# Performance work log

Hardware: AMD Instinct MI355X
Metric: run time of the kernel (lower is better)

The kernel has to match this reference:

```python
import jax, jax.numpy as jnp
import numpy as np

B, T, L_CTX = 64, 150, 256
H = 512   # decoder_num_hidden
E = 512   # target_embedding_size
V = 1000  # target_vocab_size


def setup_inputs() -> dict:
    key = jax.random.key(0)
    ks = jax.random.split(key, 10)
    s = 0.05
    return {
        "cnn_feats": jax.random.normal(ks[0], (B, L_CTX, H), dtype=jnp.float32),
        "seq": jax.random.randint(ks[1], (B, T), 0, V, dtype=jnp.int32),
        "embed_table": jax.random.normal(ks[2], (V, E), dtype=jnp.float32) * s,
        "W_ih": jax.random.normal(ks[3], (4 * H, E), dtype=jnp.float32) * s,
        "b_ih": jnp.zeros((4 * H,), dtype=jnp.float32),
        "W_hh": jax.random.normal(ks[4], (4 * H, H), dtype=jnp.float32) * s,
        "b_hh": jnp.zeros((4 * H,), dtype=jnp.float32),
        "W_hm": jax.random.normal(ks[5], (H, H), dtype=jnp.float32) * s,
        "W_om": jax.random.normal(ks[6], (H, 2 * H), dtype=jnp.float32) * s,
        "W_logit": jax.random.normal(ks[7], (V, H), dtype=jnp.float32) * s,
        "b_logit": jnp.zeros((V,), dtype=jnp.float32),
    }


def reference(cnn_feats, seq, embed_table, W_ih, b_ih, W_hh, b_hh,
              W_hm, W_om, W_logit, b_logit):
    # Single-layer LSTMCell decoder with per-step attention (eval mode, dropout=0).
    def step(carry, it):
        h, c = carry                      # [B,H] each
        xt = jax.nn.relu(embed_table[it])  # [B,E]
        gates = xt @ W_ih.T + b_ih + h @ W_hh.T + b_hh  # [B,4H]
        i, f, g, o = jnp.split(gates, 4, axis=1)
        c2 = jax.nn.sigmoid(f) * c + jax.nn.sigmoid(i) * jnp.tanh(g)
        h2 = jax.nn.sigmoid(o) * jnp.tanh(c2)
        mapped = h2 @ W_hm.T              # [B,H]
        attn = jnp.einsum("blh,bh->bl", cnn_feats, mapped)
        w = jax.nn.softmax(attn, axis=1)
        ctx = jnp.einsum("bl,blh->bh", w, cnn_feats)
        out = jnp.concatenate([ctx, h2], axis=1) @ W_om.T  # [B,H]
        logp = jax.nn.log_softmax(out @ W_logit.T + b_logit, axis=1)
        return (h2, c2), logp

    bsz = cnn_feats.shape[0]
    h0 = jnp.zeros((bsz, W_hh.shape[1]), dtype=cnn_feats.dtype)
    c0 = jnp.zeros_like(h0)
    _, outs = jax.lax.scan(step, (h0, c0), seq.T)  # outs: [T,B,V]
    return outs.transpose(1, 0, 2)  # [B,T,V]
```

## Files before the change

### kernel.cpp

```cpp
#include <hip/hip_runtime.h>
#include <math.h>

#define B_  64
#define T_  150
#define L_  256
#define H_  512
#define E_  512
#define V_  1000
#define G4_ 2048
#define DB_ 16
#define HCB 32

typedef _Float16 f16;
typedef f16   f16x8 __attribute__((ext_vector_type(8)));
typedef f16   f16x4 __attribute__((ext_vector_type(4)));
typedef float f32x4 __attribute__((ext_vector_type(4)));
typedef unsigned long long ull;

__device__ __forceinline__ float sigmf(float x) { return 1.0f / (1.0f + expf(-x)); }

__global__ __launch_bounds__(512) void decoder_mfma(
    const int*   __restrict__ seq,
    const float* __restrict__ G,
    const float* __restrict__ Whh,
    ull*  __restrict__ xh,
    int*  __restrict__ tags,
    float* __restrict__ hbuf)
{
    __shared__ f16   hlds[64][520];
    __shared__ float glds[64][132];
    __shared__ float csh[64][36];

    const int tid = threadIdx.x;
    const int bb  = blockIdx.x;
    const int ln  = tid & 63;
    const int wv  = tid >> 6;
    const int mh  = wv >> 2;
    const int nt2 = wv & 3;

    f16x8 bfr[2][16];
    #pragma unroll
    for (int j = 0; j < 2; ++j) {
        const int n = 2 * nt2 + j;
        const int grow = (n >> 1) * H_ + bb * HCB + (n & 1) * 16 + (ln & 15);
        #pragma unroll
        for (int kt = 0; kt < 16; ++kt) {
            const int k0 = kt * 32 + (ln >> 4) * 8;
            float4 w0 = *(const float4*)(Whh + (size_t)grow * H_ + k0);
            float4 w1 = *(const float4*)(Whh + (size_t)grow * H_ + k0 + 4);
            bfr[j][kt] = (f16x8){(f16)w0.x, (f16)w0.y, (f16)w0.z, (f16)w0.w,
                                 (f16)w1.x, (f16)w1.y, (f16)w1.z, (f16)w1.w};
        }
    }
    for (int e = tid; e < 64 * 520 / 4; e += 512) ((ull*)hlds)[e] = 0ull;
    for (int e = tid; e < 64 * 36; e += 512) ((float*)csh)[e] = 0.f;
    __syncthreads();

    const int cb = tid >> 3, cg = tid & 7;

    for (int t = 0; t < T_; ++t) {
        const int v = seq[cb * T_ + t];
        const float* gp = G + (size_t)v * G4_ + bb * HCB + cg * 4;
        float4 gq0 = *(const float4*)(gp);
        float4 gq1 = *(const float4*)(gp + H_);
        float4 gq2 = *(const float4*)(gp + 2 * H_);
        float4 gq3 = *(const float4*)(gp + 3 * H_);

        if (t > 0) {
            if (tid < DB_) {
                while (__hip_atomic_load(&tags[tid], __ATOMIC_RELAXED,
                                         __HIP_MEMORY_SCOPE_AGENT) < t) {}
            }
            __syncthreads();
            const ull* src = xh + (size_t)(t & 1) * 64 * 128;
            ull v0[8], v1[8];
            #pragma unroll
            for (int it = 0; it < 8; ++it) {
                const int e = tid + it * 512;
                const int b = e >> 6, s = e & 63;
                v0[it] = __hip_atomic_load(&src[b * 128 + 2 * s], __ATOMIC_RELAXED,
                                           __HIP_MEMORY_SCOPE_AGENT);
                v1[it] = __hip_atomic_load(&src[b * 128 + 2 * s + 1], __ATOMIC_RELAXED,
                                           __HIP_MEMORY_SCOPE_AGENT);
            }
            #pragma unroll
            for (int it = 0; it < 8; ++it) {
                const int e = tid + it * 512;
                const int b = e >> 6, s = e & 63;
                ull* dst = (ull*)&hlds[b][s * 8];
                dst[0] = v0[it]; dst[1] = v1[it];
            }
            __syncthreads();
        }

        f32x4 acc00 = {0.f,0.f,0.f,0.f}, acc01 = {0.f,0.f,0.f,0.f};
        f32x4 acc10 = {0.f,0.f,0.f,0.f}, acc11 = {0.f,0.f,0.f,0.f};
        #pragma unroll
        for (int kt = 0; kt < 16; ++kt) {
            const int ko = kt * 32 + (ln >> 4) * 8;
            f16x8 a0 = *(const f16x8*)&hlds[(2 * mh)     * 16 + (ln & 15)][ko];
            f16x8 a1 = *(const f16x8*)&hlds[(2 * mh + 1) * 16 + (ln & 15)][ko];
            acc00 = __builtin_amdgcn_mfma_f32_16x16x32_f16(a0, bfr[0][kt], acc00, 0, 0, 0);
            acc01 = __builtin_amdgcn_mfma_f32_16x16x32_f16(a0, bfr[1][kt], acc01, 0, 0, 0);
            acc10 = __builtin_amdgcn_mfma_f32_16x16x32_f16(a1, bfr[0][kt], acc10, 0, 0, 0);
            acc11 = __builtin_amdgcn_mfma_f32_16x16x32_f16(a1, bfr[1][kt], acc11, 0, 0, 0);
        }
        {
            const int r0 = (2 * mh) * 16 + (ln >> 4) * 4;
            const int r1 = (2 * mh + 1) * 16 + (ln >> 4) * 4;
            const int c0 = (2 * nt2) * 16 + (ln & 15);
            const int c1 = (2 * nt2 + 1) * 16 + (ln & 15);
            #pragma unroll
            for (int i = 0; i < 4; ++i) {
                glds[r0 + i][c0] = acc00[i];
                glds[r0 + i][c1] = acc01[i];
                glds[r1 + i][c0] = acc10[i];
                glds[r1 + i][c1] = acc11[i];
            }
        }
        __syncthreads();

        {
            float4 Gi = *(const float4*)&glds[cb][cg * 4];
            float4 Gf = *(const float4*)&glds[cb][32 + cg * 4];
            float4 Gg = *(const float4*)&glds[cb][64 + cg * 4];
            float4 Go = *(const float4*)&glds[cb][96 + cg * 4];
            float4 cold = *(const float4*)&csh[cb][cg * 4];
            float gi[4] = {Gi.x + gq0.x, Gi.y + gq0.y, Gi.z + gq0.z, Gi.w + gq0.w};
            float gf[4] = {Gf.x + gq1.x, Gf.y + gq1.y, Gf.z + gq1.z, Gf.w + gq1.w};
            float gg[4] = {Gg.x + gq2.x, Gg.y + gq2.y, Gg.z + gq2.z, Gg.w + gq2.w};
            float go[4] = {Go.x + gq3.x, Go.y + gq3.y, Go.z + gq3.z, Go.w + gq3.w};
            float cl[4] = {cold.x, cold.y, cold.z, cold.w};
            float4 cnew, hnew;
            f16x4 hp;
            #pragma unroll
            for (int i = 0; i < 4; ++i) {
                float c2 = sigmf(gf[i]) * cl[i] + sigmf(gi[i]) * tanhf(gg[i]);
                float h2 = sigmf(go[i]) * tanhf(c2);
                ((float*)&cnew)[i] = c2;
                ((float*)&hnew)[i] = h2;
                hp[i] = (f16)h2;
            }
            *(float4*)&csh[cb][cg * 4] = cnew;
            *(float4*)&hbuf[((size_t)t * 64 + cb) * H_ + bb * HCB + cg * 4] = hnew;
            __hip_atomic_store(
                &xh[(size_t)((t + 1) & 1) * 64 * 128 + cb * 128 + bb * 8 + cg],
                __builtin_bit_cast(ull, hp),
                __ATOMIC_RELAXED, __HIP_MEMORY_SCOPE_AGENT);
        }
        __syncthreads();
        if (tid == 0)
            __hip_atomic_store(&tags[bb], t + 1, __ATOMIC_RELAXED,
                               __HIP_MEMORY_SCOPE_AGENT);
    }
}

template<bool RELU_A, bool REMAP>
__global__ __launch_bounds__(256) void gemm16_nt(
    const float* __restrict__ A1, const float* __restrict__ A2,
    const float* __restrict__ Bm,
    const float* __restrict__ bias1, const float* __restrict__ bias2,
    float* __restrict__ C, int M, int N, int KA)
{
    __shared__ f16 As[64][40];
    __shared__ f16 Bs[64][40];
    const int tid = threadIdx.x;
    const int m0 = blockIdx.x * 64, n0 = blockIdx.y * 64;
    const int ln = tid & 63, wv = tid >> 6;
    const int lr = tid >> 2, lc8 = (tid & 3) * 8;
    const int K = A2 ? 2 * KA : KA;
    f32x4 acc[4] = {};

    for (int kb = 0; kb < K; kb += 32) {
        const float* Ap; int kk;
        if (kb < KA) { Ap = A1; kk = kb; } else { Ap = A2; kk = kb - KA; }
        int gm = m0 + lr;
        float4 a0 = make_float4(0.f, 0.f, 0.f, 0.f), a1 = a0;
        if (gm < M) {
            a0 = *(const float4*)(Ap + (size_t)gm * KA + kk + lc8);
            a1 = *(const float4*)(Ap + (size_t)gm * KA + kk + lc8 + 4);
        }
        if (RELU_A) {
            a0.x = fmaxf(a0.x, 0.f); a0.y = fmaxf(a0.y, 0.f);
            a0.z = fmaxf(a0.z, 0.f); a0.w = fmaxf(a0.w, 0.f);
            a1.x = fmaxf(a1.x, 0.f); a1.y = fmaxf(a1.y, 0.f);
            a1.z = fmaxf(a1.z, 0.f); a1.w = fmaxf(a1.w, 0.f);
        }
        f16x8 av = {(f16)a0.x, (f16)a0.y, (f16)a0.z, (f16)a0.w,
                    (f16)a1.x, (f16)a1.y, (f16)a1.z, (f16)a1.w};
        *(f16x8*)&As[lr][lc8] = av;

        int gn = n0 + lr;
        float4 b0 = make_float4(0.f, 0.f, 0.f, 0.f), b1 = b0;
        if (gn < N) {
            b0 = *(const float4*)(Bm + (size_t)gn * K + kb + lc8);
            b1 = *(const float4*)(Bm + (size_t)gn * K + kb + lc8 + 4);
        }
        f16x8 bv = {(f16)b0.x, (f16)b0.y, (f16)b0.z, (f16)b0.w,
                    (f16)b1.x, (f16)b1.y, (f16)b1.z, (f16)b1.w};
        *(f16x8*)&Bs[lr][lc8] = bv;
        __syncthreads();

        f16x8 af = *(const f16x8*)&As[wv * 16 + (ln & 15)][(ln >> 4) * 8];
        #pragma unroll
        for (int ntt = 0; ntt < 4; ++ntt) {
            f16x8 bf = *(const f16x8*)&Bs[ntt * 16 + (ln & 15)][(ln >> 4) * 8];
            acc[ntt] = __builtin_amdgcn_mfma_f32_16x16x32_f16(af, bf, acc[ntt], 0, 0, 0);
        }
        __syncthreads();
    }

    #pragma unroll
    for (int ntt = 0; ntt < 4; ++ntt) {
        #pragma unroll
        for (int i = 0; i < 4; ++i) {
            int gm = m0 + wv * 16 + (ln >> 4) * 4 + i;
            int gn = n0 + ntt * 16 + (ln & 15);
            if (gm < M && gn < N) {
                float v = acc[ntt][i];
                if (bias1) v += bias1[gn];
                if (bias2) v += bias2[gn];
                size_t row = REMAP ? ((size_t)(gm & 63) * T_ + (gm >> 6)) : (size_t)gm;
                C[row * (size_t)N + gn] = v;
            }
        }
    }
}

__global__ __launch_bounds__(256) void gemm_nt(
    const float* __restrict__ A, size_t lda, size_t azs,
    const float* __restrict__ Bm, size_t ldb, size_t bzs,
    float* __restrict__ C, size_t ldc, size_t czs, int M, int N, int K)
{
    A  += blockIdx.z * azs;
    Bm += blockIdx.z * bzs;
    C  += blockIdx.z * czs;
    __shared__ __align__(16) float As[16][68];
    __shared__ __align__(16) float Bs[16][68];
    const int tid = threadIdx.x;
    const int m0 = blockIdx.x * 64;
    const int n0 = blockIdx.y * 64;
    const int lr = tid >> 2;
    const int lc = (tid & 3) << 2;
    const int tm = (tid & 15) << 2;
    const int tn = (tid >> 4) << 2;
    float acc[4][4] = {};

    for (int kb = 0; kb < K; kb += 16) {
        float4 a4 = make_float4(0.f, 0.f, 0.f, 0.f);
        int gm = m0 + lr;
        if (gm < M) a4 = *(const float4*)(A + (size_t)gm * lda + kb + lc);
        As[lc + 0][lr] = a4.x; As[lc + 1][lr] = a4.y;
        As[lc + 2][lr] = a4.z; As[lc + 3][lr] = a4.w;

        float4 b4 = make_float4(0.f, 0.f, 0.f, 0.f);
        int gn = n0 + lr;
        if (gn < N) b4 = *(const float4*)(Bm + (size_t)gn * ldb + kb + lc);
        Bs[lc + 0][lr] = b4.x; Bs[lc + 1][lr] = b4.y;
        Bs[lc + 2][lr] = b4.z; Bs[lc + 3][lr] = b4.w;
        __syncthreads();

        #pragma unroll
        for (int k = 0; k < 16; ++k) {
            float4 av = *(const float4*)&As[k][tm];
            float4 bv = *(const float4*)&Bs[k][tn];
            float af[4] = {av.x, av.y, av.z, av.w};
            float bf[4] = {bv.x, bv.y, bv.z, bv.w};
            #pragma unroll
            for (int i = 0; i < 4; ++i)
                #pragma unroll
                for (int j = 0; j < 4; ++j)
                    acc[i][j] += af[i] * bf[j];
        }
        __syncthreads();
    }

    #pragma unroll
    for (int i = 0; i < 4; ++i) {
        int gm = m0 + tm + i;
        if (gm >= M) continue;
        #pragma unroll
        for (int j = 0; j < 4; ++j) {
            int gn = n0 + tn + j;
            if (gn >= N) continue;
            C[(size_t)gm * ldc + gn] = acc[i][j];
        }
    }
}

__global__ __launch_bounds__(256) void gemm_nn(
    const float* __restrict__ A, size_t lda, size_t azs,
    const float* __restrict__ Bm, size_t ldb, size_t bzs,
    float* __restrict__ C, size_t ldc, size_t czs, int M, int N, int K)
{
    A  += blockIdx.z * azs;
    Bm += blockIdx.z * bzs;
    C  += blockIdx.z * czs;
    __shared__ __align__(16) float As[16][68];
    __shared__ __align__(16) float Bs[16][68];
    const int tid = threadIdx.x;
    const int m0 = blockIdx.x * 64;
    const int n0 = blockIdx.y * 64;
    const int lr = tid >> 2;
    const int lc = (tid & 3) << 2;
    const int br = tid >> 4;
    const int bc = (tid & 15) << 2;
    const int tm = (tid & 15) << 2;
    const int tn = (tid >> 4) << 2;
    float acc[4][4] = {};

    for (int kb = 0; kb < K; kb += 16) {
        float4 a4 = make_float4(0.f, 0.f, 0.f, 0.f);
        int gm = m0 + lr;
        if (gm < M) a4 = *(const float4*)(A + (size_t)gm * lda + kb + lc);
        As[lc + 0][lr] = a4.x; As[lc + 1][lr] = a4.y;
        As[lc + 2][lr] = a4.z; As[lc + 3][lr] = a4.w;

        float4 b4 = make_float4(0.f, 0.f, 0.f, 0.f);
        if (n0 + bc < N) b4 = *(const float4*)(Bm + (size_t)(kb + br) * ldb + n0 + bc);
        Bs[br][bc + 0] = b4.x; Bs[br][bc + 1] = b4.y;
        Bs[br][bc + 2] = b4.z; Bs[br][bc + 3] = b4.w;
        __syncthreads();

        #pragma unroll
        for (int k = 0; k < 16; ++k) {
            float4 av = *(const float4*)&As[k][tm];
            float4 bv = *(const float4*)&Bs[k][tn];
            float af[4] = {av.x, av.y, av.z, av.w};
            float bf[4] = {bv.x, bv.y, bv.z, bv.w};
            #pragma unroll
            for (int i = 0; i < 4; ++i)
                #pragma unroll
                for (int j = 0; j < 4; ++j)
                    acc[i][j] += af[i] * bf[j];
        }
        __syncthreads();
    }

    #pragma unroll
    for (int i = 0; i < 4; ++i) {
        int gm = m0 + tm + i;
        if (gm >= M) continue;
        #pragma unroll
        for (int j = 0; j < 4; ++j) {
            int gn = n0 + tn + j;
            if (gn >= N) continue;
            C[(size_t)gm * ldc + gn] = acc[i][j];
        }
    }
}

__global__ __launch_bounds__(256) void att_softmax(float* __restrict__ att, int nrows)
{
    const int tid = threadIdx.x, lane = tid & 63, wave = tid >> 6;
    const int row = blockIdx.x * 4 + wave;
    if (row >= nrows) return;
    float4* p = (float4*)(att + (size_t)row * L_);
    float4 sc = p[lane];
    float mx = fmaxf(fmaxf(sc.x, sc.y), fmaxf(sc.z, sc.w));
    #pragma unroll
    for (int off = 32; off; off >>= 1) mx = fmaxf(mx, __shfl_xor(mx, off));
    float e0 = expf(sc.x - mx), e1 = expf(sc.y - mx);
    float e2 = expf(sc.z - mx), e3 = expf(sc.w - mx);
    float s = e0 + e1 + e2 + e3;
    #pragma unroll
    for (int off = 32; off; off >>= 1) s += __shfl_xor(s, off);
    float inv = 1.f / s;
    p[lane] = make_float4(e0 * inv, e1 * inv, e2 * inv, e3 * inv);
}

__global__ __launch_bounds__(256) void logsoftmax_k(float* __restrict__ out)
{
    const int row = blockIdx.x;
    float* p = out + (size_t)row * V_;
    const int tid = threadIdx.x, lane = tid & 63, wave = tid >> 6;
    __shared__ float red[8];

    float vals[4];
    int n = 0;
    float mx = -INFINITY;
    for (int v = tid; v < V_; v += 256) { vals[n] = p[v]; mx = fmaxf(mx, vals[n]); ++n; }
    #pragma unroll
    for (int off = 32; off; off >>= 1) mx = fmaxf(mx, __shfl_xor(mx, off));
    if (lane == 0) red[wave] = mx;
    __syncthreads();
    mx = fmaxf(fmaxf(red[0], red[1]), fmaxf(red[2], red[3]));

    float s = 0.f;
    for (int i = 0; i < n; ++i) s += expf(vals[i] - mx);
    #pragma unroll
    for (int off = 32; off; off >>= 1) s += __shfl_xor(s, off);
    if (lane == 0) red[4 + wave] = s;
    __syncthreads();
    s = red[4] + red[5] + red[6] + red[7];

    const float lse = mx + logf(s);
    n = 0;
    for (int v = tid; v < V_; v += 256) { p[v] = vals[n] - lse; ++n; }
}

extern "C" void kernel_launch(void* const* d_in, const int* in_sizes, int n_in,
                              void* d_out, int out_size, void* d_ws, size_t ws_size,
                              hipStream_t stream)
{
    const float* cnn     = (const float*)d_in[0];
    const int*   seq     = (const int*)d_in[1];
    const float* embed   = (const float*)d_in[2];
    const float* W_ih    = (const float*)d_in[3];
    const float* b_ih    = (const float*)d_in[4];
    const float* W_hh    = (const float*)d_in[5];
    const float* b_hh    = (const float*)d_in[6];
    const float* W_hm    = (const float*)d_in[7];
    const float* W_om    = (const float*)d_in[8];
    const float* W_logit = (const float*)d_in[9];
    const float* b_logit = (const float*)d_in[10];
    float* out = (float*)d_out;

    float* ws = (float*)d_ws;
    float* G    = ws;
    float* hbuf = G + (size_t)V_ * G4_;
    float* outv = hbuf + (size_t)B_ * T_ * H_;
    ull*   xh   = (ull*)(outv + (size_t)B_ * T_ * H_);
    int*   tags = (int*)(xh + 2 * 64 * 128);
    float* mapped = out;
    float* attb   = out + (size_t)B_ * T_ * H_;

    hipMemsetAsync(tags, 0, DB_ * sizeof(int), stream);

    gemm16_nt<true, false><<<dim3(16, 32), 256, 0, stream>>>(
        embed, nullptr, W_ih, b_ih, b_hh, G, V_, G4_, E_);

    decoder_mfma<<<DB_, 512, 0, stream>>>(seq, G, W_hh, xh, tags, hbuf);

    gemm16_nt<false, false><<<dim3(150, 8), 256, 0, stream>>>(
        hbuf, nullptr, W_hm, nullptr, nullptr, mapped, B_ * T_, H_, H_);
    gemm_nt<<<dim3(3, 4, 64), 256, 0, stream>>>(
        mapped, (size_t)B_ * H_, H_,
        cnn, H_, (size_t)L_ * H_,
        attb, L_, (size_t)T_ * L_, T_, L_, H_);
    att_softmax<<<(B_ * T_ + 3) / 4, 256, 0, stream>>>(attb, B_ * T_);
    gemm_nn<<<dim3(3, 8, 64), 256, 0, stream>>>(
        attb, L_, (size_t)T_ * L_,
        cnn, H_, (size_t)L_ * H_,
        mapped, (size_t)B_ * H_, H_, T_, H_, L_);
    gemm16_nt<false, false><<<dim3(150, 8), 256, 0, stream>>>(
        mapped, hbuf, W_om, nullptr, nullptr, outv, B_ * T_, H_, H_);
    gemm16_nt<false, true><<<dim3(150, 16), 256, 0, stream>>>(
        outv, nullptr, W_logit, b_logit, nullptr, out, B_ * T_, V_, H_);
    logsoftmax_k<<<B_ * T_, 256, 0, stream>>>(out);
}
```

Measured before the change: 1.078 ms.

## Use sc1 vector loads for hidden exchange and MFMA for attention scores

The recurrent decoder now exchanges the fp16 hidden state through 16-byte global loads and stores carrying the sc1 cache modifier, replacing pairs of 8-byte relaxed atomics. The LSTM cell update is remapped to 256 threads handling 8 elements each, so each thread issues wider global and LDS accesses. Separately, the fp32 SIMT batched GEMM that computes the attention scores is replaced by an fp16 MFMA kernel. The aim is to shorten the per-step synchronisation latency of the serial decoder and speed up the attention-score GEMM, at the cost of reduced precision there and reliance on inline asm for cache coherence across blocks.

```diff
diff --git a/kernel.cpp b/kernel.cpp
--- a/kernel.cpp
+++ b/kernel.cpp
@@ -15,21 +15,35 @@
 typedef f16   f16x8 __attribute__((ext_vector_type(8)));
 typedef f16   f16x4 __attribute__((ext_vector_type(4)));
 typedef float f32x4 __attribute__((ext_vector_type(4)));
+typedef unsigned int u32x4 __attribute__((ext_vector_type(4)));
 typedef unsigned long long ull;
 
 __device__ __forceinline__ float sigmf(float x) { return 1.0f / (1.0f + expf(-x)); }
+
+__device__ __forceinline__ u32x4 load16_sc1(const void* p)
+{
+    u32x4 r;
+    asm volatile("global_load_dwordx4 %0, %1, off sc1"
+                 : "=v"(r) : "v"(p) : "memory");
+    return r;
+}
+__device__ __forceinline__ void store16_sc1(void* p, u32x4 v)
+{
+    asm volatile("global_store_dwordx4 %0, %1, off sc1"
+                 :: "v"(p), "v"(v) : "memory");
+}
 
 __global__ __launch_bounds__(512) void decoder_mfma(
     const int*   __restrict__ seq,
     const float* __restrict__ G,
     const float* __restrict__ Whh,
-    ull*  __restrict__ xh,
+    f16*  __restrict__ xh,
     int*  __restrict__ tags,
     float* __restrict__ hbuf)
 {
-    __shared__ f16   hlds[64][520];
-    __shared__ float glds[64][132];
-    __shared__ float csh[64][36];
+    __shared__ __align__(16) f16   hlds[64][520];
+    __shared__ __align__(16) float glds[64][132];
+    __shared__ __align__(16) float csh[64][36];
 
     const int tid = threadIdx.x;
     const int bb  = blockIdx.x;
@@ -56,15 +70,19 @@
     for (int e = tid; e < 64 * 36; e += 512) ((float*)csh)[e] = 0.f;
     __syncthreads();
 
-    const int cb = tid >> 3, cg = tid & 7;
+    const int cb = tid >> 2, cg = tid & 3;
 
     for (int t = 0; t < T_; ++t) {
-        const int v = seq[cb * T_ + t];
-        const float* gp = G + (size_t)v * G4_ + bb * HCB + cg * 4;
-        float4 gq0 = *(const float4*)(gp);
-        float4 gq1 = *(const float4*)(gp + H_);
-        float4 gq2 = *(const float4*)(gp + 2 * H_);
-        float4 gq3 = *(const float4*)(gp + 3 * H_);
+        float4 ga[4][2];
+        if (tid < 256) {
+            const int v = seq[cb * T_ + t];
+            const float* gp = G + (size_t)v * G4_ + bb * HCB + cg * 8;
+            #pragma unroll
+            for (int q = 0; q < 4; ++q) {
+                ga[q][0] = *(const float4*)(gp + q * H_);
+                ga[q][1] = *(const float4*)(gp + q * H_ + 4);
+            }
+        }
 
         if (t > 0) {
             if (tid < DB_) {
@@ -72,23 +90,20 @@
                                          __HIP_MEMORY_SCOPE_AGENT) < t) {}
             }
             __syncthreads();
-            const ull* src = xh + (size_t)(t & 1) * 64 * 128;
-            ull v0[8], v1[8];
+            const f16* src = xh + (size_t)(t & 1) * 64 * 512;
+            u32x4 vv[8];
             #pragma unroll
             for (int it = 0; it < 8; ++it) {
                 const int e = tid + it * 512;
                 const int b = e >> 6, s = e & 63;
-                v0[it] = __hip_atomic_load(&src[b * 128 + 2 * s], __ATOMIC_RELAXED,
-                                           __HIP_MEMORY_SCOPE_AGENT);
-                v1[it] = __hip_atomic_load(&src[b * 128 + 2 * s + 1], __ATOMIC_RELAXED,
-                                           __HIP_MEMORY_SCOPE_AGENT);
-            }
+                vv[it] = load16_sc1(src + b * 512 + s * 8);
+            }
+            asm volatile("s_waitcnt vmcnt(0)" ::: "memory");
             #pragma unroll
             for (int it = 0; it < 8; ++it) {
                 const int e = tid + it * 512;
                 const int b = e >> 6, s = e & 63;
-                ull* dst = (ull*)&hlds[b][s * 8];
-                dst[0] = v0[it]; dst[1] = v1[it];
+                *(u32x4*)&hlds[b][s * 8] = vv[it];
             }
             __syncthreads();
         }
@@ -120,33 +135,39 @@
         }
         __syncthreads();
 
-        {
-            float4 Gi = *(const float4*)&glds[cb][cg * 4];
-            float4 Gf = *(const float4*)&glds[cb][32 + cg * 4];
-            float4 Gg = *(const float4*)&glds[cb][64 + cg * 4];
-            float4 Go = *(const float4*)&glds[cb][96 + cg * 4];
-            float4 cold = *(const float4*)&csh[cb][cg * 4];
-            float gi[4] = {Gi.x + gq0.x, Gi.y + gq0.y, Gi.z + gq0.z, Gi.w + gq0.w};
-            float gf[4] = {Gf.x + gq1.x, Gf.y + gq1.y, Gf.z + gq1.z, Gf.w + gq1.w};
-            float gg[4] = {Gg.x + gq2.x, Gg.y + gq2.y, Gg.z + gq2.z, Gg.w + gq2.w};
-            float go[4] = {Go.x + gq3.x, Go.y + gq3.y, Go.z + gq3.z, Go.w + gq3.w};
-            float cl[4] = {cold.x, cold.y, cold.z, cold.w};
-            float4 cnew, hnew;
-            f16x4 hp;
-            #pragma unroll
-            for (int i = 0; i < 4; ++i) {
+        if (tid < 256) {
+            float gi[8], gf[8], gg[8], go[8], cl[8];
+            #pragma unroll
+            for (int hh = 0; hh < 2; ++hh) {
+                float4 Gi = *(const float4*)&glds[cb][cg * 8 + hh * 4];
+                float4 Gf = *(const float4*)&glds[cb][32 + cg * 8 + hh * 4];
+                float4 Gg = *(const float4*)&glds[cb][64 + cg * 8 + hh * 4];
+                float4 Go = *(const float4*)&glds[cb][96 + cg * 8 + hh * 4];
+                float4 cc = *(const float4*)&csh[cb][cg * 8 + hh * 4];
+                #pragma unroll
+                for (int i = 0; i < 4; ++i) {
+                    gi[hh * 4 + i] = ((const float*)&Gi)[i] + ((const float*)&ga[0][hh])[i];
+                    gf[hh * 4 + i] = ((const float*)&Gf)[i] + ((const float*)&ga[1][hh])[i];
+                    gg[hh * 4 + i] = ((const float*)&Gg)[i] + ((const float*)&ga[2][hh])[i];
+                    go[hh * 4 + i] = ((const float*)&Go)[i] + ((const float*)&ga[3][hh])[i];
+                    cl[hh * 4 + i] = ((const float*)&cc)[i];
+                }
+            }
+            float hv[8], cv[8];
+            f16x8 hp;
+            #pragma unroll
+            for (int i = 0; i < 8; ++i) {
                 float c2 = sigmf(gf[i]) * cl[i] + sigmf(gi[i]) * tanhf(gg[i]);
                 float h2 = sigmf(go[i]) * tanhf(c2);
-                ((float*)&cnew)[i] = c2;
-                ((float*)&hnew)[i] = h2;
-                hp[i] = (f16)h2;
-            }
-            *(float4*)&csh[cb][cg * 4] = cnew;
-            *(float4*)&hbuf[((size_t)t * 64 + cb) * H_ + bb * HCB + cg * 4] = hnew;
-            __hip_atomic_store(
-                &xh[(size_t)((t + 1) & 1) * 64 * 128 + cb * 128 + bb * 8 + cg],
-                __builtin_bit_cast(ull, hp),
-                __ATOMIC_RELAXED, __HIP_MEMORY_SCOPE_AGENT);
+                cv[i] = c2; hv[i] = h2; hp[i] = (f16)h2;
+            }
+            *(float4*)&csh[cb][cg * 8]     = make_float4(cv[0], cv[1], cv[2], cv[3]);
+            *(float4*)&csh[cb][cg * 8 + 4] = make_float4(cv[4], cv[5], cv[6], cv[7]);
+            float* hb = hbuf + ((size_t)t * 64 + cb) * H_ + bb * HCB + cg * 8;
+            *(float4*)hb       = make_float4(hv[0], hv[1], hv[2], hv[3]);
+            *(float4*)(hb + 4) = make_float4(hv[4], hv[5], hv[6], hv[7]);
+            store16_sc1(xh + (size_t)((t + 1) & 1) * 64 * 512 + cb * 512 + bb * HCB + cg * 8,
+                        __builtin_bit_cast(u32x4, hp));
         }
         __syncthreads();
         if (tid == 0)
@@ -211,7 +232,7 @@
     }
 
     #pragma unroll
-    for (int ntt = 0; ntt < 4; ++ntt) {
+    for (int ntt = 0; ntt < 4; ++ntt)
         #pragma unroll
         for (int i = 0; i < 4; ++i) {
             int gm = m0 + wv * 16 + (ln >> 4) * 4 + i;
@@ -224,10 +245,9 @@
                 C[row * (size_t)N + gn] = v;
             }
         }
-    }
-}
-
-__global__ __launch_bounds__(256) void gemm_nt(
+}
+
+__global__ __launch_bounds__(256) void gemm16_bt(
     const float* __restrict__ A, size_t lda, size_t azs,
     const float* __restrict__ Bm, size_t ldb, size_t bzs,
     float* __restrict__ C, size_t ldc, size_t czs, int M, int N, int K)
@@ -235,57 +255,54 @@
     A  += blockIdx.z * azs;
     Bm += blockIdx.z * bzs;
     C  += blockIdx.z * czs;
-    __shared__ __align__(16) float As[16][68];
-    __shared__ __align__(16) float Bs[16][68];
+    __shared__ f16 As[64][40];
+    __shared__ f16 Bs[64][40];
     const int tid = threadIdx.x;
-    const int m0 = blockIdx.x * 64;
-    const int n0 = blockIdx.y * 64;
-    const int lr = tid >> 2;
-    const int lc = (tid & 3) << 2;
-    const int tm = (tid & 15) << 2;
-    const int tn = (tid >> 4) << 2;
-    float acc[4][4] = {};
-
-    for (int kb = 0; kb < K; kb += 16) {
-        float4 a4 = make_float4(0.f, 0.f, 0.f, 0.f);
+    const int m0 = blockIdx.x * 64, n0 = blockIdx.y * 64;
+    const int ln = tid & 63, wv = tid >> 6;
+    const int lr = tid >> 2, lc8 = (tid & 3) * 8;
+    f32x4 acc[4] = {};
+
+    for (int kb = 0; kb < K; kb += 32) {
         int gm = m0 + lr;
-        if (gm < M) a4 = *(const float4*)(A + (size_t)gm * lda + kb + lc);
-        As[lc + 0][lr] = a4.x; As[lc + 1][lr] = a4.y;
-        As[lc + 2][lr] = a4.z; As[lc + 3][lr] = a4.w;
-
-        float4 b4 = make_float4(0.f, 0.f, 0.f, 0.f);
+        float4 a0 = make_float4(0.f, 0.f, 0.f, 0.f), a1 = a0;
+        if (gm < M) {
+            a0 = *(const float4*)(A + (size_t)gm * lda + kb + lc8);
+            a1 = *(const float4*)(A + (size_t)gm * lda + kb + lc8 + 4);
+        }
+        f16x8 av = {(f16)a0.x, (f16)a0.y, (f16)a0.z, (f16)a0.w,
+                    (f16)a1.x, (f16)a1.y, (f16)a1.z, (f16)a1.w};
+        *(f16x8*)&As[lr][lc8] = av;
+
         int gn = n0 + lr;
-        if (gn < N) b4 = *(const float4*)(Bm + (size_t)gn * ldb + kb + lc);
-        Bs[lc + 0][lr] = b4.x; Bs[lc + 1][lr] = b4.y;
-        Bs[lc + 2][lr] = b4.z; Bs[lc + 3][lr] = b4.w;
-        __syncthreads();
-
-        #pragma unroll
-        for (int k = 0; k < 16; ++k) {
-            float4 av = *(const float4*)&As[k][tm];
-            float4 bv = *(const float4*)&Bs[k][tn];
-            float af[4] = {av.x, av.y, av.z, av.w};
-            float bf[4] = {bv.x, bv.y, bv.z, bv.w};
-            #pragma unroll
-            for (int i = 0; i < 4; ++i)
-                #pragma unroll
-                for (int j = 0; j < 4; ++j)
-                    acc[i][j] += af[i] * bf[j];
-        }
-        __syncthreads();
-    }
-
-    #pragma unroll
-    for (int i = 0; i < 4; ++i) {
-        int gm = m0 + tm + i;
-        if (gm >= M) continue;
-        #pragma unroll
-        for (int j = 0; j < 4; ++j) {
-            int gn = n0 + tn + j;
-            if (gn >= N) continue;
-            C[(size_t)gm * ldc + gn] = acc[i][j];
-        }
-    }
+        float4 b0 = make_float4(0.f, 0.f, 0.f, 0.f), b1 = b0;
+        if (gn < N) {
+            b0 = *(const float4*)(Bm + (size_t)gn * ldb + kb + lc8);
+            b1 = *(const float4*)(Bm + (size_t)gn * ldb + kb + lc8 + 4);
+        }
+        f16x8 bv = {(f16)b0.x, (f16)b0.y, (f16)b0.z, (f16)b0.w,
+                    (f16)b1.x, (f16)b1.y, (f16)b1.z, (f16)b1.w};
+        *(f16x8*)&Bs[lr][lc8] = bv;
+        __syncthreads();
+
+        f16x8 af = *(const f16x8*)&As[wv * 16 + (ln & 15)][(ln >> 4) * 8];
+        #pragma unroll
+        for (int ntt = 0; ntt < 4; ++ntt) {
+            f16x8 bf = *(const f16x8*)&Bs[ntt * 16 + (ln & 15)][(ln >> 4) * 8];
+            acc[ntt] = __builtin_amdgcn_mfma_f32_16x16x32_f16(af, bf, acc[ntt], 0, 0, 0);
+        }
+        __syncthreads();
+    }
+
+    #pragma unroll
+    for (int ntt = 0; ntt < 4; ++ntt)
+        #pragma unroll
+        for (int i = 0; i < 4; ++i) {
+            int gm = m0 + wv * 16 + (ln >> 4) * 4 + i;
+            int gn = n0 + ntt * 16 + (ln & 15);
+            if (gm < M && gn < N)
+                C[(size_t)gm * ldc + gn] = acc[ntt][i];
+        }
 }
 
 __global__ __launch_bounds__(256) void gemm_nn(
@@ -420,8 +437,8 @@
     float* G    = ws;
     float* hbuf = G + (size_t)V_ * G4_;
     float* outv = hbuf + (size_t)B_ * T_ * H_;
-    ull*   xh   = (ull*)(outv + (size_t)B_ * T_ * H_);
-    int*   tags = (int*)(xh + 2 * 64 * 128);
+    f16*   xh   = (f16*)(outv + (size_t)B_ * T_ * H_);
+    int*   tags = (int*)(xh + 2 * 64 * 512);
     float* mapped = out;
     float* attb   = out + (size_t)B_ * T_ * H_;
 
@@ -434,7 +451,7 @@
 
     gemm16_nt<false, false><<<dim3(150, 8), 256, 0, stream>>>(
         hbuf, nullptr, W_hm, nullptr, nullptr, mapped, B_ * T_, H_, H_);
-    gemm_nt<<<dim3(3, 4, 64), 256, 0, stream>>>(
+    gemm16_bt<<<dim3(3, 4, 64), 256, 0, stream>>>(
         mapped, (size_t)B_ * H_, H_,
         cnn, H_, (size_t)L_ * H_,
         attb, L_, (size_t)T_ * L_, T_, L_, H_);
```

After: 1.080 ms. About the same (+0.2%).

## Fuse attention scores with softmax and move attention GEMMs to fp16 MFMA

Applied to the files above, without the earlier changes.

Replaces the fp32 scalar batched score GEMM and the separate softmax kernel with one kernel. It computes a 64x256 score tile per (t-block, batch) with f16 MFMA, applies the row softmax in shared memory, and writes probabilities as fp16. The context GEMM also becomes an f16 MFMA kernel that reads the fp16 probabilities and transposes cnn features into LDS. This removes the fp32 score round-trip, one kernel launch, and the slow FMA loops, at the cost of fp16 rounding of scores, probabilities and features, plus heavy shared memory use in the fused kernel.

```diff
diff --git a/kernel.cpp b/kernel.cpp
--- a/kernel.cpp
+++ b/kernel.cpp
@@ -211,7 +211,7 @@
     }
 
     #pragma unroll
-    for (int ntt = 0; ntt < 4; ++ntt) {
+    for (int ntt = 0; ntt < 4; ++ntt)
         #pragma unroll
         for (int i = 0; i < 4; ++i) {
             int gm = m0 + wv * 16 + (ln >> 4) * 4 + i;
@@ -224,149 +224,148 @@
                 C[row * (size_t)N + gn] = v;
             }
         }
-    }
-}
-
-__global__ __launch_bounds__(256) void gemm_nt(
-    const float* __restrict__ A, size_t lda, size_t azs,
-    const float* __restrict__ Bm, size_t ldb, size_t bzs,
-    float* __restrict__ C, size_t ldc, size_t czs, int M, int N, int K)
-{
-    A  += blockIdx.z * azs;
-    Bm += blockIdx.z * bzs;
-    C  += blockIdx.z * czs;
-    __shared__ __align__(16) float As[16][68];
-    __shared__ __align__(16) float Bs[16][68];
+}
+
+__global__ __launch_bounds__(512) void score_softmax(
+    const float* __restrict__ mapped,
+    const float* __restrict__ cnn,
+    f16* __restrict__ attP)
+{
+    __shared__ f16   As[64][40];
+    __shared__ f16   Bs[256][40];
+    __shared__ float sl[64][260];
+
     const int tid = threadIdx.x;
-    const int m0 = blockIdx.x * 64;
-    const int n0 = blockIdx.y * 64;
-    const int lr = tid >> 2;
-    const int lc = (tid & 3) << 2;
-    const int tm = (tid & 15) << 2;
-    const int tn = (tid >> 4) << 2;
-    float acc[4][4] = {};
-
-    for (int kb = 0; kb < K; kb += 16) {
-        float4 a4 = make_float4(0.f, 0.f, 0.f, 0.f);
-        int gm = m0 + lr;
-        if (gm < M) a4 = *(const float4*)(A + (size_t)gm * lda + kb + lc);
-        As[lc + 0][lr] = a4.x; As[lc + 1][lr] = a4.y;
-        As[lc + 2][lr] = a4.z; As[lc + 3][lr] = a4.w;
-
-        float4 b4 = make_float4(0.f, 0.f, 0.f, 0.f);
-        int gn = n0 + lr;
-        if (gn < N) b4 = *(const float4*)(Bm + (size_t)gn * ldb + kb + lc);
-        Bs[lc + 0][lr] = b4.x; Bs[lc + 1][lr] = b4.y;
-        Bs[lc + 2][lr] = b4.z; Bs[lc + 3][lr] = b4.w;
-        __syncthreads();
-
-        #pragma unroll
-        for (int k = 0; k < 16; ++k) {
-            float4 av = *(const float4*)&As[k][tm];
-            float4 bv = *(const float4*)&Bs[k][tn];
-            float af[4] = {av.x, av.y, av.z, av.w};
-            float bf[4] = {bv.x, bv.y, bv.z, bv.w};
+    const int m0  = blockIdx.x * 64;
+    const int b   = blockIdx.y;
+    const int ln  = tid & 63, wv = tid >> 6;
+    const int mh  = wv >> 2, nq = wv & 3;
+    const int ln15 = ln & 15, ln4 = (ln >> 4) * 8;
+    const float* cnnb = cnn + (size_t)b * L_ * H_;
+
+    f32x4 acc[2][4] = {};
+
+    for (int kb = 0; kb < H_; kb += 32) {
+        {
+            int lr = tid >> 3, lc4 = (tid & 7) * 4;
+            int t = m0 + lr;
+            float4 a = make_float4(0.f, 0.f, 0.f, 0.f);
+            if (t < T_) a = *(const float4*)(mapped + ((size_t)t * 64 + b) * H_ + kb + lc4);
+            As[lr][lc4 + 0] = (f16)a.x; As[lr][lc4 + 1] = (f16)a.y;
+            As[lr][lc4 + 2] = (f16)a.z; As[lr][lc4 + 3] = (f16)a.w;
+        }
+        {
+            int br = tid >> 1, bc16 = (tid & 1) * 16;
+            const float* src = cnnb + (size_t)br * H_ + kb + bc16;
+            float4 w0 = *(const float4*)(src);
+            float4 w1 = *(const float4*)(src + 4);
+            float4 w2 = *(const float4*)(src + 8);
+            float4 w3 = *(const float4*)(src + 12);
+            f16x8 p0 = {(f16)w0.x, (f16)w0.y, (f16)w0.z, (f16)w0.w,
+                        (f16)w1.x, (f16)w1.y, (f16)w1.z, (f16)w1.w};
+            f16x8 p1 = {(f16)w2.x, (f16)w2.y, (f16)w2.z, (f16)w2.w,
+                        (f16)w3.x, (f16)w3.y, (f16)w3.z, (f16)w3.w};
+            *(f16x8*)&Bs[br][bc16]     = p0;
+            *(f16x8*)&Bs[br][bc16 + 8] = p1;
+        }
+        __syncthreads();
+
+        f16x8 a0 = *(const f16x8*)&As[(2 * mh)     * 16 + ln15][ln4];
+        f16x8 a1 = *(const f16x8*)&As[(2 * mh + 1) * 16 + ln15][ln4];
+        #pragma unroll
+        for (int nj = 0; nj < 4; ++nj) {
+            f16x8 bf = *(const f16x8*)&Bs[(nq * 4 + nj) * 16 + ln15][ln4];
+            acc[0][nj] = __builtin_amdgcn_mfma_f32_16x16x32_f16(a0, bf, acc[0][nj], 0, 0, 0);
+            acc[1][nj] = __builtin_amdgcn_mfma_f32_16x16x32_f16(a1, bf, acc[1][nj], 0, 0, 0);
+        }
+        __syncthreads();
+    }
+
+    #pragma unroll
+    for (int mi = 0; mi < 2; ++mi)
+        #pragma unroll
+        for (int nj = 0; nj < 4; ++nj)
             #pragma unroll
             for (int i = 0; i < 4; ++i)
-                #pragma unroll
-                for (int j = 0; j < 4; ++j)
-                    acc[i][j] += af[i] * bf[j];
-        }
-        __syncthreads();
-    }
-
-    #pragma unroll
-    for (int i = 0; i < 4; ++i) {
-        int gm = m0 + tm + i;
-        if (gm >= M) continue;
-        #pragma unroll
-        for (int j = 0; j < 4; ++j) {
-            int gn = n0 + tn + j;
-            if (gn >= N) continue;
-            C[(size_t)gm * ldc + gn] = acc[i][j];
-        }
-    }
-}
-
-__global__ __launch_bounds__(256) void gemm_nn(
-    const float* __restrict__ A, size_t lda, size_t azs,
-    const float* __restrict__ Bm, size_t ldb, size_t bzs,
-    float* __restrict__ C, size_t ldc, size_t czs, int M, int N, int K)
-{
-    A  += blockIdx.z * azs;
-    Bm += blockIdx.z * bzs;
-    C  += blockIdx.z * czs;
-    __shared__ __align__(16) float As[16][68];
-    __shared__ __align__(16) float Bs[16][68];
+                sl[(2 * mh + mi) * 16 + (ln >> 4) * 4 + i][(nq * 4 + nj) * 16 + ln15]
+                    = acc[mi][nj][i];
+    __syncthreads();
+
+    #pragma unroll
+    for (int rr = 0; rr < 8; ++rr) {
+        int r = wv * 8 + rr;
+        int t = m0 + r;
+        if (t < T_) {
+            float4 v = *(const float4*)&sl[r][ln * 4];
+            float mx = fmaxf(fmaxf(v.x, v.y), fmaxf(v.z, v.w));
+            #pragma unroll
+            for (int off = 32; off; off >>= 1) mx = fmaxf(mx, __shfl_xor(mx, off));
+            float e0 = expf(v.x - mx), e1 = expf(v.y - mx);
+            float e2 = expf(v.z - mx), e3 = expf(v.w - mx);
+            float s = e0 + e1 + e2 + e3;
+            #pragma unroll
+            for (int off = 32; off; off >>= 1) s += __shfl_xor(s, off);
+            float inv = 1.f / s;
+            f16x4 p = {(f16)(e0 * inv), (f16)(e1 * inv), (f16)(e2 * inv), (f16)(e3 * inv)};
+            *(f16x4*)(attP + ((size_t)b * T_ + t) * L_ + ln * 4) = p;
+        }
+    }
+}
+
+__global__ __launch_bounds__(256) void ctx16_nn(
+    const f16* __restrict__ attP,
+    const float* __restrict__ cnn,
+    float* __restrict__ ctxout)
+{
+    __shared__ f16 As[64][40];
+    __shared__ f16 Bs[64][40];
     const int tid = threadIdx.x;
-    const int m0 = blockIdx.x * 64;
-    const int n0 = blockIdx.y * 64;
-    const int lr = tid >> 2;
-    const int lc = (tid & 3) << 2;
-    const int br = tid >> 4;
-    const int bc = (tid & 15) << 2;
-    const int tm = (tid & 15) << 2;
-    const int tn = (tid >> 4) << 2;
-    float acc[4][4] = {};
-
-    for (int kb = 0; kb < K; kb += 16) {
-        float4 a4 = make_float4(0.f, 0.f, 0.f, 0.f);
-        int gm = m0 + lr;
-        if (gm < M) a4 = *(const float4*)(A + (size_t)gm * lda + kb + lc);
-        As[lc + 0][lr] = a4.x; As[lc + 1][lr] = a4.y;
-        As[lc + 2][lr] = a4.z; As[lc + 3][lr] = a4.w;
-
-        float4 b4 = make_float4(0.f, 0.f, 0.f, 0.f);
-        if (n0 + bc < N) b4 = *(const float4*)(Bm + (size_t)(kb + br) * ldb + n0 + bc);
-        Bs[br][bc + 0] = b4.x; Bs[br][bc + 1] = b4.y;
-        Bs[br][bc + 2] = b4.z; Bs[br][bc + 3] = b4.w;
-        __syncthreads();
-
-        #pragma unroll
-        for (int k = 0; k < 16; ++k) {
-            float4 av = *(const float4*)&As[k][tm];
-            float4 bv = *(const float4*)&Bs[k][tn];
-            float af[4] = {av.x, av.y, av.z, av.w};
-            float bf[4] = {bv.x, bv.y, bv.z, bv.w};
-            #pragma unroll
-            for (int i = 0; i < 4; ++i)
-                #pragma unroll
-                for (int j = 0; j < 4; ++j)
-                    acc[i][j] += af[i] * bf[j];
-        }
-        __syncthreads();
-    }
-
-    #pragma unroll
-    for (int i = 0; i < 4; ++i) {
-        int gm = m0 + tm + i;
-        if (gm >= M) continue;
-        #pragma unroll
-        for (int j = 0; j < 4; ++j) {
-            int gn = n0 + tn + j;
-            if (gn >= N) continue;
-            C[(size_t)gm * ldc + gn] = acc[i][j];
-        }
-    }
-}
-
-__global__ __launch_bounds__(256) void att_softmax(float* __restrict__ att, int nrows)
-{
-    const int tid = threadIdx.x, lane = tid & 63, wave = tid >> 6;
-    const int row = blockIdx.x * 4 + wave;
-    if (row >= nrows) return;
-    float4* p = (float4*)(att + (size_t)row * L_);
-    float4 sc = p[lane];
-    float mx = fmaxf(fmaxf(sc.x, sc.y), fmaxf(sc.z, sc.w));
-    #pragma unroll
-    for (int off = 32; off; off >>= 1) mx = fmaxf(mx, __shfl_xor(mx, off));
-    float e0 = expf(sc.x - mx), e1 = expf(sc.y - mx);
-    float e2 = expf(sc.z - mx), e3 = expf(sc.w - mx);
-    float s = e0 + e1 + e2 + e3;
-    #pragma unroll
-    for (int off = 32; off; off >>= 1) s += __shfl_xor(s, off);
-    float inv = 1.f / s;
-    p[lane] = make_float4(e0 * inv, e1 * inv, e2 * inv, e3 * inv);
+    const int m0 = blockIdx.x * 64, n0 = blockIdx.y * 64;
+    const int b  = blockIdx.z;
+    const int ln = tid & 63, wv = tid >> 6;
+    const int ln15 = ln & 15, ln4 = (ln >> 4) * 8;
+    const float* cnnb = cnn + (size_t)b * L_ * H_;
+    const f16*   pb   = attP + (size_t)b * T_ * L_;
+    f32x4 acc[4] = {};
+
+    for (int kb = 0; kb < L_; kb += 32) {
+        {
+            int lr = tid >> 2, lc8 = (tid & 3) * 8;
+            int t = m0 + lr;
+            f16x8 av = {};
+            if (t < T_) av = *(const f16x8*)(pb + (size_t)t * L_ + kb + lc8);
+            *(f16x8*)&As[lr][lc8] = av;
+        }
+        {
+            int br = tid >> 3;
+            int nc = (tid & 7) * 8;
+            const float* src = cnnb + (size_t)(kb + br) * H_ + n0 + nc;
+            float4 w0 = *(const float4*)(src);
+            float4 w1 = *(const float4*)(src + 4);
+            float wv8[8] = {w0.x, w0.y, w0.z, w0.w, w1.x, w1.y, w1.z, w1.w};
+            #pragma unroll
+            for (int j = 0; j < 8; ++j) Bs[nc + j][br] = (f16)wv8[j];
+        }
+        __syncthreads();
+
+        f16x8 af = *(const f16x8*)&As[wv * 16 + ln15][ln4];
+        #pragma unroll
+        for (int ntt = 0; ntt < 4; ++ntt) {
+            f16x8 bf = *(const f16x8*)&Bs[ntt * 16 + ln15][ln4];
+            acc[ntt] = __builtin_amdgcn_mfma_f32_16x16x32_f16(af, bf, acc[ntt], 0, 0, 0);
+        }
+        __syncthreads();
+    }
+
+    #pragma unroll
+    for (int ntt = 0; ntt < 4; ++ntt)
+        #pragma unroll
+        for (int i = 0; i < 4; ++i) {
+            int t  = m0 + wv * 16 + (ln >> 4) * 4 + i;
+            int gn = n0 + ntt * 16 + ln15;
+            if (t < T_)
+                ctxout[(size_t)b * H_ + (size_t)t * (B_ * H_) + gn] = acc[ntt][i];
+        }
 }
 
 __global__ __launch_bounds__(256) void logsoftmax_k(float* __restrict__ out)
@@ -423,7 +422,7 @@
     ull*   xh   = (ull*)(outv + (size_t)B_ * T_ * H_);
     int*   tags = (int*)(xh + 2 * 64 * 128);
     float* mapped = out;
-    float* attb   = out + (size_t)B_ * T_ * H_;
+    f16*   attP   = (f16*)(out + (size_t)B_ * T_ * H_);
 
     hipMemsetAsync(tags, 0, DB_ * sizeof(int), stream);
 
@@ -434,15 +433,8 @@
 
     gemm16_nt<false, false><<<dim3(150, 8), 256, 0, stream>>>(
         hbuf, nullptr, W_hm, nullptr, nullptr, mapped, B_ * T_, H_, H_);
-    gemm_nt<<<dim3(3, 4, 64), 256, 0, stream>>>(
-        mapped, (size_t)B_ * H_, H_,
-        cnn, H_, (size_t)L_ * H_,
-        attb, L_, (size_t)T_ * L_, T_, L_, H_);
-    att_softmax<<<(B_ * T_ + 3) / 4, 256, 0, stream>>>(attb, B_ * T_);
-    gemm_nn<<<dim3(3, 8, 64), 256, 0, stream>>>(
-        attb, L_, (size_t)T_ * L_,
-        cnn, H_, (size_t)L_ * H_,
-        mapped, (size_t)B_ * H_, H_, T_, H_, L_);
+    score_softmax<<<dim3(3, 64), 512, 0, stream>>>(mapped, cnn, attP);
+    ctx16_nn<<<dim3(3, 8, 64), 256, 0, stream>>>(attP, cnn, mapped);
     gemm16_nt<false, false><<<dim3(150, 8), 256, 0, stream>>>(
         mapped, hbuf, W_om, nullptr, nullptr, outv, B_ * T_, H_, H_);
     gemm16_nt<false, true><<<dim3(150, 16), 256, 0, stream>>>(
```

Result: faster. 1.021 ms (median of 2 runs) (-5.3%).
